# Kernel optimization log

Measured on AMD Instinct MI355X. Metric: run time of the kernel, lower is better.

The kernel has to match this reference:

```python
import jax, jax.numpy as jnp
import numpy as np

N_HEAD = 8  # heads; per-head scores are summed before softmax


def setup_inputs() -> dict:
    key = jax.random.key(0)
    k1, k2, k3 = jax.random.split(key, 3)
    B, T, D = 4, 512, 1024
    N, H = 16, 256  # n_concepts, init_size
    x = jax.random.normal(k1, (B, T, D), dtype=jnp.float32)
    # original init: kaiming_uniform then / d_model**2 -> very small weights; plain normal scaled similarly
    w_qs = jax.random.normal(k2, (N, D, H), dtype=jnp.float32) / (D ** 1.0)
    w_ks = jax.random.normal(k3, (N, D, H), dtype=jnp.float32) / (D ** 1.0)
    return {"x": x, "w_qs": w_qs, "w_ks": w_ks}


def reference(x, w_qs, w_ks):
    # x: [B,T,D]; w_qs/w_ks: [N,D,H]
    # Faithful to source: k_list is built from wq (source bug), so scores = q.q^T; w_ks unused in math.
    wq = jnp.einsum('btd,ndh->bnth', x, w_qs)  # [B,N,T,H]
    # Per-head split then sum over heads of q_h @ k_h^T equals the full-H contraction
    # (mask is None), so fuse: sum_h qk_h == wq @ wq^T over the whole H axis.
    attn = jnp.einsum('bnsh,bnth->bnst', wq, wq)  # temperature = 1.0; head-sum fused
    attn = jax.nn.softmax(attn, axis=-1)  # [B,N,T,T]
    # input = x.unsqueeze(1): [B,1,T,D]; einsum 'bnst,bitd->bnsd' broadcasts i=1
    e_aggregated = jnp.einsum('bnst,btd->bnsd', attn, x)  # [B,N,T,D]
    return e_aggregated, attn
```

## Files before the change

kernel.cpp:

```cpp
#include <hip/hip_runtime.h>
#include <hip/hip_bf16.h>

typedef __bf16 bf16x8 __attribute__((ext_vector_type(8)));
typedef unsigned short u16x8 __attribute__((ext_vector_type(8)));
typedef float f32x4 __attribute__((ext_vector_type(4)));
typedef __hip_bfloat16 hbf;

static constexpr int B = 4, T = 512, D = 1024, N = 16, H = 256;
static constexpr size_t E_ELEMS = (size_t)B * N * T * D;
static constexpr size_t ATTN_ELEMS = (size_t)B * N * T * T;

__device__ __forceinline__ bf16x8 load8(const hbf* p) {
  return *reinterpret_cast<const bf16x8*>(p);
}

__device__ __forceinline__ unsigned short f2bf(float f) {
  union { __hip_bfloat16 h; unsigned short u; } cv;
  cv.h = __float2bfloat16(f);
  return cv.u;
}

__device__ __forceinline__ void gload16(const hbf* g, hbf* l) {
  __builtin_amdgcn_global_load_lds(
      (const __attribute__((address_space(1))) void*)g,
      (__attribute__((address_space(3))) void*)l, 16, 0, 0);
}

__global__ __launch_bounds__(256) void cast_bf_k(const float* __restrict__ in,
                                                 unsigned short* __restrict__ out,
                                                 int n8) {
  int i = blockIdx.x * 256 + threadIdx.x;
  if (i >= n8) return;
  const float4* p = reinterpret_cast<const float4*>(in) + (size_t)i * 2;
  float4 a = p[0], b = p[1];
  u16x8 v;
  v[0] = f2bf(a.x); v[1] = f2bf(a.y); v[2] = f2bf(a.z); v[3] = f2bf(a.w);
  v[4] = f2bf(b.x); v[5] = f2bf(b.y); v[6] = f2bf(b.z); v[7] = f2bf(b.w);
  reinterpret_cast<u16x8*>(out)[i] = v;
}

__global__ void transpose_cast_k(const float* __restrict__ in,
                                 unsigned short* __restrict__ out, int R, int C) {
  __shared__ unsigned short tile[32][33];
  int z = blockIdx.z;
  int c0 = blockIdx.x * 32, r0 = blockIdx.y * 32;
  const float* inz = in + (size_t)z * R * C;
  unsigned short* outz = out + (size_t)z * R * C;
  int tx = threadIdx.x, ty = threadIdx.y;
  for (int i = ty; i < 32; i += 8)
    tile[i][tx] = f2bf(inz[(size_t)(r0 + i) * C + (c0 + tx)]);
  __syncthreads();
  for (int i = ty; i < 32; i += 8)
    outz[(size_t)(c0 + i) * R + (r0 + tx)] = tile[tx][i];
}

__global__ __launch_bounds__(256) void gemm_wq_tiled(const hbf* __restrict__ xb,
                                                     const hbf* __restrict__ wT,
                                                     hbf* __restrict__ wq) {
  __shared__ __align__(16) hbf As[128 * 32];
  __shared__ __align__(16) hbf Bs[128 * 32];
  int idx = blockIdx.x;
  int b = idx >> 7, mt = (idx >> 5) & 3, jt = idx & 31;
  const hbf* A = xb + (size_t)b * T * D + (size_t)mt * 128 * D;
  const hbf* Bp = wT + (size_t)jt * 128 * D;
  int tid = threadIdx.x, wave = tid >> 6, lane = tid & 63;
  int col = lane & 15, quad = lane >> 4;
  int wm = wave & 1, wn = wave >> 1;
  const hbf* stG = (wave < 2) ? A : Bp;
  hbf* stL = (wave < 2) ? As : Bs;
  int ibase = (wave & 1) * 4;
  f32x4 acc[4][4] = {};
  for (int k0 = 0; k0 < D; k0 += 32) {
    __syncthreads();
#pragma unroll
    for (int j = 0; j < 4; ++j) {
      int slot = (ibase + j) * 64 + lane;
      int row = slot >> 2, kc = slot & 3;
      gload16(stG + (size_t)row * D + k0 + kc * 8, stL + slot * 8);
    }
    __syncthreads();
    bf16x8 a[4], bb[4];
#pragma unroll
    for (int s = 0; s < 4; ++s)
      a[s] = load8(As + (wm * 64 + s * 16 + col) * 32 + quad * 8);
#pragma unroll
    for (int t = 0; t < 4; ++t)
      bb[t] = load8(Bs + (wn * 64 + t * 16 + col) * 32 + quad * 8);
#pragma unroll
    for (int s = 0; s < 4; ++s)
#pragma unroll
      for (int t = 0; t < 4; ++t)
        acc[s][t] = __builtin_amdgcn_mfma_f32_16x16x32_bf16(a[s], bb[t], acc[s][t], 0, 0, 0);
  }
  hbf* wqb = wq + (size_t)b * 16 * T * H;
#pragma unroll
  for (int s = 0; s < 4; ++s) {
    int row = mt * 128 + wm * 64 + s * 16 + quad * 4;
#pragma unroll
    for (int t = 0; t < 4; ++t) {
      int j = jt * 128 + wn * 64 + t * 16 + col;
      int n = j >> 8, h = j & 255;
      hbf* dst = wqb + (size_t)n * T * H + (size_t)row * H + h;
#pragma unroll
      for (int r = 0; r < 4; ++r)
        dst[(size_t)r * H] = __float2bfloat16(acc[s][t][r]);
    }
  }
}

__global__ __launch_bounds__(256) void attn_k(const hbf* __restrict__ wq,
                                              float* __restrict__ attn_f,
                                              hbf* __restrict__ attn_b) {
  __shared__ float S[16][516];
  int blk = blockIdx.x;
  int bn = blk >> 5;
  int mt = blk & 31;
  const hbf* Wq = wq + (size_t)bn * T * H;
  int wave = threadIdx.x >> 6, lane = threadIdx.x & 63;
  int col = lane & 15, quad = lane >> 4;
  int m0 = mt * 16;
  f32x4 acc[8] = {};
  for (int k0 = 0; k0 < H; k0 += 32) {
    int k = k0 + quad * 8;
    bf16x8 afrag = load8(Wq + (size_t)(m0 + col) * H + k);
#pragma unroll
    for (int t = 0; t < 8; ++t) {
      int jrow = wave * 128 + t * 16 + col;
      bf16x8 bfrag = load8(Wq + (size_t)jrow * H + k);
      acc[t] = __builtin_amdgcn_mfma_f32_16x16x32_bf16(afrag, bfrag, acc[t], 0, 0, 0);
    }
  }
#pragma unroll
  for (int t = 0; t < 8; ++t)
#pragma unroll
    for (int r = 0; r < 4; ++r)
      S[quad * 4 + r][wave * 128 + t * 16 + col] = acc[t][r];
  __syncthreads();
  for (int rr = 0; rr < 4; ++rr) {
    int row = wave * 4 + rr;
    float v[8];
    float mx = -1e30f;
#pragma unroll
    for (int i = 0; i < 8; ++i) { v[i] = S[row][lane + i * 64]; mx = fmaxf(mx, v[i]); }
#pragma unroll
    for (int off = 32; off > 0; off >>= 1) mx = fmaxf(mx, __shfl_xor(mx, off));
    float sum = 0.f;
#pragma unroll
    for (int i = 0; i < 8; ++i) { v[i] = __expf(v[i] - mx); sum += v[i]; }
#pragma unroll
    for (int off = 32; off > 0; off >>= 1) sum += __shfl_xor(sum, off);
    float inv = 1.0f / sum;
    size_t base = ((size_t)bn * T + m0 + row) * T;
    float* dst = attn_f + base;
    hbf* dstb = attn_b + base;
#pragma unroll
    for (int i = 0; i < 8; ++i) {
      float p = v[i] * inv;
      dst[lane + i * 64] = p;
      dstb[lane + i * 64] = __float2bfloat16(p);
    }
  }
}

__global__ __launch_bounds__(256) void gemm_out_tiled(const hbf* __restrict__ attn,
                                                      const hbf* __restrict__ xT,
                                                      float* __restrict__ eout) {
  __shared__ __align__(16) hbf As[128 * 32];
  __shared__ __align__(16) hbf Bs[128 * 32];
  int idx = blockIdx.x;
  int bn = idx >> 5, mt = (idx >> 3) & 3, nt = idx & 7;
  int b = bn >> 4;
  const hbf* A = attn + (size_t)bn * T * T + (size_t)mt * 128 * T;
  const hbf* Bp = xT + (size_t)b * D * T + (size_t)nt * 128 * T;
  float* C = eout + (size_t)bn * T * D;
  int tid = threadIdx.x, wave = tid >> 6, lane = tid & 63;
  int col = lane & 15, quad = lane >> 4;
  int wm = wave & 1, wn = wave >> 1;
  const hbf* stG = (wave < 2) ? A : Bp;
  hbf* stL = (wave < 2) ? As : Bs;
  int ibase = (wave & 1) * 4;
  f32x4 acc[4][4] = {};
  for (int k0 = 0; k0 < T; k0 += 32) {
    __syncthreads();
#pragma unroll
    for (int j = 0; j < 4; ++j) {
      int slot = (ibase + j) * 64 + lane;
      int row = slot >> 2, kc = slot & 3;
      gload16(stG + (size_t)row * T + k0 + kc * 8, stL + slot * 8);
    }
    __syncthreads();
    bf16x8 a[4], bb[4];
#pragma unroll
    for (int s = 0; s < 4; ++s)
      a[s] = load8(As + (wm * 64 + s * 16 + col) * 32 + quad * 8);
#pragma unroll
    for (int t = 0; t < 4; ++t)
      bb[t] = load8(Bs + (wn * 64 + t * 16 + col) * 32 + quad * 8);
#pragma unroll
    for (int s = 0; s < 4; ++s)
#pragma unroll
      for (int t = 0; t < 4; ++t)
        acc[s][t] = __builtin_amdgcn_mfma_f32_16x16x32_bf16(a[s], bb[t], acc[s][t], 0, 0, 0);
  }
#pragma unroll
  for (int s = 0; s < 4; ++s) {
    int row = mt * 128 + wm * 64 + s * 16 + quad * 4;
#pragma unroll
    for (int t = 0; t < 4; ++t) {
      int d = nt * 128 + wn * 64 + t * 16 + col;
      float* dst = C + (size_t)row * D + d;
#pragma unroll
      for (int r = 0; r < 4; ++r)
        dst[(size_t)r * D] = acc[s][t][r];
    }
  }
}

extern "C" void kernel_launch(void* const* d_in, const int* in_sizes, int n_in,
                              void* d_out, int out_size, void* d_ws, size_t ws_size,
                              hipStream_t stream) {
  const float* x = (const float*)d_in[0];
  const float* w_qs = (const float*)d_in[1];
  float* e_out = (float*)d_out;
  float* attn_out = e_out + E_ELEMS;

  char* ws = (char*)d_ws;
  hbf* x_bf = (hbf*)ws;
  hbf* xT   = (hbf*)(ws + (4u << 20));
  hbf* wT   = (hbf*)(ws + (8u << 20));
  hbf* wq   = (hbf*)(ws + (16u << 20));
  hbf* attn_b = (hbf*)(ws + (32u << 20));

  dim3 tb(32, 8);
  cast_bf_k<<<1024, 256, 0, stream>>>(x, (unsigned short*)x_bf, (B * T * D) / 8);
  transpose_cast_k<<<dim3(H / 32, D / 32, N), tb, 0, stream>>>(
      w_qs, (unsigned short*)wT, D, H);
  transpose_cast_k<<<dim3(D / 32, T / 32, B), tb, 0, stream>>>(
      x, (unsigned short*)xT, T, D);
  gemm_wq_tiled<<<512, 256, 0, stream>>>(x_bf, wT, wq);
  attn_k<<<2048, 256, 0, stream>>>(wq, attn_out, attn_b);
  gemm_out_tiled<<<2048, 256, 0, stream>>>(attn_b, xT, e_out);
}
```

Before: 364.9 us.

## Fuse softmax attention with PV matmul, keeping probabilities in swizzled LDS

Merges the score/softmax kernel and the attn@x GEMM into one kernel. Each block computes 32 query rows, runs the softmax in registers with cross-wave reductions through shared memory, and keeps the bf16 probabilities in XOR-swizzled LDS, then multiplies them by xT streamed straight from global memory. This removes the bf16 attention round trip through global memory and one launch. In exchange, the PV stage reads B fragments directly from global without LDS staging and uses fewer, heavier blocks with a 32KB LDS footprint.

```diff
diff --git a/kernel.cpp b/kernel.cpp
--- a/kernel.cpp
+++ b/kernel.cpp
@@ -108,111 +108,122 @@
   }
 }
 
-__global__ __launch_bounds__(256) void attn_k(const hbf* __restrict__ wq,
-                                              float* __restrict__ attn_f,
-                                              hbf* __restrict__ attn_b) {
-  __shared__ float S[16][516];
+__global__ __launch_bounds__(256) void attn_pv_fused(
+    const hbf* __restrict__ wq, const hbf* __restrict__ xT,
+    float* __restrict__ attn_f, float* __restrict__ eout) {
+  __shared__ __align__(16) char Pl[32 * 512 * 2];
+  __shared__ float redA[4][32];
+  __shared__ float redB[4][32];
   int blk = blockIdx.x;
-  int bn = blk >> 5;
-  int mt = blk & 31;
+  int bn = blk >> 4, mt = blk & 15;
+  int b = bn >> 4;
+  int m0 = mt * 32;
   const hbf* Wq = wq + (size_t)bn * T * H;
   int wave = threadIdx.x >> 6, lane = threadIdx.x & 63;
   int col = lane & 15, quad = lane >> 4;
-  int m0 = mt * 16;
-  f32x4 acc[8] = {};
+
+  f32x4 acc[2][8] = {};
   for (int k0 = 0; k0 < H; k0 += 32) {
     int k = k0 + quad * 8;
-    bf16x8 afrag = load8(Wq + (size_t)(m0 + col) * H + k);
+    bf16x8 af[2];
+#pragma unroll
+    for (int s = 0; s < 2; ++s)
+      af[s] = load8(Wq + (size_t)(m0 + s * 16 + col) * H + k);
 #pragma unroll
     for (int t = 0; t < 8; ++t) {
-      int jrow = wave * 128 + t * 16 + col;
-      bf16x8 bfrag = load8(Wq + (size_t)jrow * H + k);
-      acc[t] = __builtin_amdgcn_mfma_f32_16x16x32_bf16(afrag, bfrag, acc[t], 0, 0, 0);
-    }
-  }
-#pragma unroll
-  for (int t = 0; t < 8; ++t)
-#pragma unroll
-    for (int r = 0; r < 4; ++r)
-      S[quad * 4 + r][wave * 128 + t * 16 + col] = acc[t][r];
-  __syncthreads();
-  for (int rr = 0; rr < 4; ++rr) {
-    int row = wave * 4 + rr;
-    float v[8];
-    float mx = -1e30f;
-#pragma unroll
-    for (int i = 0; i < 8; ++i) { v[i] = S[row][lane + i * 64]; mx = fmaxf(mx, v[i]); }
-#pragma unroll
-    for (int off = 32; off > 0; off >>= 1) mx = fmaxf(mx, __shfl_xor(mx, off));
-    float sum = 0.f;
-#pragma unroll
-    for (int i = 0; i < 8; ++i) { v[i] = __expf(v[i] - mx); sum += v[i]; }
-#pragma unroll
-    for (int off = 32; off > 0; off >>= 1) sum += __shfl_xor(sum, off);
-    float inv = 1.0f / sum;
-    size_t base = ((size_t)bn * T + m0 + row) * T;
-    float* dst = attn_f + base;
-    hbf* dstb = attn_b + base;
-#pragma unroll
-    for (int i = 0; i < 8; ++i) {
-      float p = v[i] * inv;
-      dst[lane + i * 64] = p;
-      dstb[lane + i * 64] = __float2bfloat16(p);
-    }
-  }
-}
-
-__global__ __launch_bounds__(256) void gemm_out_tiled(const hbf* __restrict__ attn,
-                                                      const hbf* __restrict__ xT,
-                                                      float* __restrict__ eout) {
-  __shared__ __align__(16) hbf As[128 * 32];
-  __shared__ __align__(16) hbf Bs[128 * 32];
-  int idx = blockIdx.x;
-  int bn = idx >> 5, mt = (idx >> 3) & 3, nt = idx & 7;
-  int b = bn >> 4;
-  const hbf* A = attn + (size_t)bn * T * T + (size_t)mt * 128 * T;
-  const hbf* Bp = xT + (size_t)b * D * T + (size_t)nt * 128 * T;
-  float* C = eout + (size_t)bn * T * D;
-  int tid = threadIdx.x, wave = tid >> 6, lane = tid & 63;
-  int col = lane & 15, quad = lane >> 4;
-  int wm = wave & 1, wn = wave >> 1;
-  const hbf* stG = (wave < 2) ? A : Bp;
-  hbf* stL = (wave < 2) ? As : Bs;
-  int ibase = (wave & 1) * 4;
-  f32x4 acc[4][4] = {};
-  for (int k0 = 0; k0 < T; k0 += 32) {
-    __syncthreads();
-#pragma unroll
-    for (int j = 0; j < 4; ++j) {
-      int slot = (ibase + j) * 64 + lane;
-      int row = slot >> 2, kc = slot & 3;
-      gload16(stG + (size_t)row * T + k0 + kc * 8, stL + slot * 8);
-    }
-    __syncthreads();
-    bf16x8 a[4], bb[4];
-#pragma unroll
-    for (int s = 0; s < 4; ++s)
-      a[s] = load8(As + (wm * 64 + s * 16 + col) * 32 + quad * 8);
-#pragma unroll
-    for (int t = 0; t < 4; ++t)
-      bb[t] = load8(Bs + (wn * 64 + t * 16 + col) * 32 + quad * 8);
-#pragma unroll
-    for (int s = 0; s < 4; ++s)
-#pragma unroll
-      for (int t = 0; t < 4; ++t)
-        acc[s][t] = __builtin_amdgcn_mfma_f32_16x16x32_bf16(a[s], bb[t], acc[s][t], 0, 0, 0);
-  }
-#pragma unroll
-  for (int s = 0; s < 4; ++s) {
-    int row = mt * 128 + wm * 64 + s * 16 + quad * 4;
-#pragma unroll
-    for (int t = 0; t < 4; ++t) {
-      int d = nt * 128 + wn * 64 + t * 16 + col;
-      float* dst = C + (size_t)row * D + d;
-#pragma unroll
-      for (int r = 0; r < 4; ++r)
-        dst[(size_t)r * D] = acc[s][t][r];
-    }
+      bf16x8 bfr = load8(Wq + (size_t)(wave * 128 + t * 16 + col) * H + k);
+#pragma unroll
+      for (int s = 0; s < 2; ++s)
+        acc[s][t] = __builtin_amdgcn_mfma_f32_16x16x32_bf16(af[s], bfr, acc[s][t], 0, 0, 0);
+    }
+  }
+
+  float mrow[2][4], inv[2][4];
+#pragma unroll
+  for (int s = 0; s < 2; ++s)
+#pragma unroll
+    for (int r = 0; r < 4; ++r) {
+      float pm = acc[s][0][r];
+#pragma unroll
+      for (int t = 1; t < 8; ++t) pm = fmaxf(pm, acc[s][t][r]);
+#pragma unroll
+      for (int off = 8; off >= 1; off >>= 1) pm = fmaxf(pm, __shfl_xor(pm, off));
+      if (col == 0) redA[wave][s * 16 + quad * 4 + r] = pm;
+    }
+  __syncthreads();
+#pragma unroll
+  for (int s = 0; s < 2; ++s)
+#pragma unroll
+    for (int r = 0; r < 4; ++r) {
+      int rl = s * 16 + quad * 4 + r;
+      mrow[s][r] = fmaxf(fmaxf(redA[0][rl], redA[1][rl]),
+                         fmaxf(redA[2][rl], redA[3][rl]));
+      float sm = 0.f;
+#pragma unroll
+      for (int t = 0; t < 8; ++t) {
+        float e = __expf(acc[s][t][r] - mrow[s][r]);
+        acc[s][t][r] = e;
+        sm += e;
+      }
+#pragma unroll
+      for (int off = 8; off >= 1; off >>= 1) sm += __shfl_xor(sm, off);
+      if (col == 0) redB[wave][rl] = sm;
+    }
+  __syncthreads();
+#pragma unroll
+  for (int s = 0; s < 2; ++s)
+#pragma unroll
+    for (int r = 0; r < 4; ++r) {
+      int rl = s * 16 + quad * 4 + r;
+      inv[s][r] = 1.0f / (redB[0][rl] + redB[1][rl] + redB[2][rl] + redB[3][rl]);
+    }
+#pragma unroll
+  for (int s = 0; s < 2; ++s)
+#pragma unroll
+    for (int r = 0; r < 4; ++r) {
+      int rl = s * 16 + quad * 4 + r;
+      float iv = inv[s][r];
+      float* dst = attn_f + ((size_t)bn * T + m0 + rl) * T;
+#pragma unroll
+      for (int t = 0; t < 8; ++t) {
+        int c = wave * 128 + t * 16 + col;
+        float p = acc[s][t][r] * iv;
+        dst[c] = p;
+        int byte = ((rl * 512 + c) * 2) ^ ((rl & 7) << 4);
+        *reinterpret_cast<hbf*>(Pl + byte) = __float2bfloat16(p);
+      }
+    }
+  __syncthreads();
+
+  const hbf* xTb = xT + (size_t)b * D * T;
+  float* Cc = eout + ((size_t)bn * T + m0) * D;
+  for (int h = 0; h < 2; ++h) {
+    int dbase = wave * 256 + h * 128;
+    f32x4 a3[2][8] = {};
+    for (int k0 = 0; k0 < T; k0 += 32) {
+      int k = k0 + quad * 8;
+      bf16x8 pf[2];
+#pragma unroll
+      for (int s = 0; s < 2; ++s) {
+        int row = s * 16 + col;
+        int byte = ((row * 512 + k) * 2) ^ ((row & 7) << 4);
+        pf[s] = *reinterpret_cast<const bf16x8*>(Pl + byte);
+      }
+#pragma unroll
+      for (int t = 0; t < 8; ++t) {
+        bf16x8 bfr = load8(xTb + (size_t)(dbase + t * 16 + col) * T + k);
+#pragma unroll
+        for (int s = 0; s < 2; ++s)
+          a3[s][t] = __builtin_amdgcn_mfma_f32_16x16x32_bf16(pf[s], bfr, a3[s][t], 0, 0, 0);
+      }
+    }
+#pragma unroll
+    for (int s = 0; s < 2; ++s)
+#pragma unroll
+      for (int t = 0; t < 8; ++t)
+#pragma unroll
+        for (int r = 0; r < 4; ++r)
+          Cc[(size_t)(s * 16 + quad * 4 + r) * D + dbase + t * 16 + col] = a3[s][t][r];
   }
 }
 
@@ -229,7 +240,6 @@
   hbf* xT   = (hbf*)(ws + (4u << 20));
   hbf* wT   = (hbf*)(ws + (8u << 20));
   hbf* wq   = (hbf*)(ws + (16u << 20));
-  hbf* attn_b = (hbf*)(ws + (32u << 20));
 
   dim3 tb(32, 8);
   cast_bf_k<<<1024, 256, 0, stream>>>(x, (unsigned short*)x_bf, (B * T * D) / 8);
@@ -238,6 +248,5 @@
   transpose_cast_k<<<dim3(D / 32, T / 32, B), tb, 0, stream>>>(
       x, (unsigned short*)xT, T, D);
   gemm_wq_tiled<<<512, 256, 0, stream>>>(x_bf, wT, wq);
-  attn_k<<<2048, 256, 0, stream>>>(wq, attn_out, attn_b);
-  gemm_out_tiled<<<2048, 256, 0, stream>>>(attn_b, xT, e_out);
-}
+  attn_pv_fused<<<1024, 256, 0, stream>>>(wq, xT, attn_out, e_out);
+}
```

New measurement: 513.3 us. +40.7%, slower.

## Triple-buffer LDS staging in both tiled GEMMs with async prefetch

Applied to the files above, without the earlier changes.

Both tiled bf16 GEMMs (x·W projection and attn·x output) move from a single LDS buffer with two barriers per k-step to a three-stage ring. Tiles k+1 and k+2 are fetched with global_load_lds while tile k is computed, and explicit vmcnt waits plus one barrier per iteration replace the old double syncthreads. The goal is to hide global load latency behind MFMA work. It triples LDS use per block, which may lower occupancy, and correctness depends on the hand-set vmcnt counts matching the number of outstanding loads.

```diff
diff --git a/kernel.cpp b/kernel.cpp
--- a/kernel.cpp
+++ b/kernel.cpp
@@ -57,8 +57,8 @@
 __global__ __launch_bounds__(256) void gemm_wq_tiled(const hbf* __restrict__ xb,
                                                      const hbf* __restrict__ wT,
                                                      hbf* __restrict__ wq) {
-  __shared__ __align__(16) hbf As[128 * 32];
-  __shared__ __align__(16) hbf Bs[128 * 32];
+  __shared__ __align__(16) hbf As[3][128 * 32];
+  __shared__ __align__(16) hbf Bs[3][128 * 32];
   int idx = blockIdx.x;
   int b = idx >> 7, mt = (idx >> 5) & 3, jt = idx & 31;
   const hbf* A = xb + (size_t)b * T * D + (size_t)mt * 128 * D;
@@ -67,25 +67,37 @@
   int col = lane & 15, quad = lane >> 4;
   int wm = wave & 1, wn = wave >> 1;
   const hbf* stG = (wave < 2) ? A : Bp;
-  hbf* stL = (wave < 2) ? As : Bs;
   int ibase = (wave & 1) * 4;
-  f32x4 acc[4][4] = {};
-  for (int k0 = 0; k0 < D; k0 += 32) {
-    __syncthreads();
+
+  auto STAGE = [&](int kt, int bi) {
+    hbf* stL = (wave < 2) ? As[bi] : Bs[bi];
 #pragma unroll
     for (int j = 0; j < 4; ++j) {
       int slot = (ibase + j) * 64 + lane;
       int row = slot >> 2, kc = slot & 3;
-      gload16(stG + (size_t)row * D + k0 + kc * 8, stL + slot * 8);
-    }
-    __syncthreads();
+      gload16(stG + (size_t)row * D + kt * 32 + kc * 8, stL + slot * 8);
+    }
+  };
+
+  f32x4 acc[4][4] = {};
+  constexpr int NT = D / 32;
+  STAGE(0, 0);
+  STAGE(1, 1);
+  for (int k = 0; k < NT; ++k) {
+    int cb = k % 3;
+    if (k == NT - 1)
+      asm volatile("s_waitcnt vmcnt(0)" ::: "memory");
+    else
+      asm volatile("s_waitcnt vmcnt(4)" ::: "memory");
+    __builtin_amdgcn_s_barrier();
+    if (k + 2 < NT) STAGE(k + 2, (k + 2) % 3);
     bf16x8 a[4], bb[4];
 #pragma unroll
     for (int s = 0; s < 4; ++s)
-      a[s] = load8(As + (wm * 64 + s * 16 + col) * 32 + quad * 8);
+      a[s] = load8(As[cb] + (wm * 64 + s * 16 + col) * 32 + quad * 8);
 #pragma unroll
     for (int t = 0; t < 4; ++t)
-      bb[t] = load8(Bs + (wn * 64 + t * 16 + col) * 32 + quad * 8);
+      bb[t] = load8(Bs[cb] + (wn * 64 + t * 16 + col) * 32 + quad * 8);
 #pragma unroll
     for (int s = 0; s < 4; ++s)
 #pragma unroll
@@ -165,8 +177,8 @@
 __global__ __launch_bounds__(256) void gemm_out_tiled(const hbf* __restrict__ attn,
                                                       const hbf* __restrict__ xT,
                                                       float* __restrict__ eout) {
-  __shared__ __align__(16) hbf As[128 * 32];
-  __shared__ __align__(16) hbf Bs[128 * 32];
+  __shared__ __align__(16) hbf As[3][128 * 32];
+  __shared__ __align__(16) hbf Bs[3][128 * 32];
   int idx = blockIdx.x;
   int bn = idx >> 5, mt = (idx >> 3) & 3, nt = idx & 7;
   int b = bn >> 4;
@@ -177,25 +189,37 @@
   int col = lane & 15, quad = lane >> 4;
   int wm = wave & 1, wn = wave >> 1;
   const hbf* stG = (wave < 2) ? A : Bp;
-  hbf* stL = (wave < 2) ? As : Bs;
   int ibase = (wave & 1) * 4;
-  f32x4 acc[4][4] = {};
-  for (int k0 = 0; k0 < T; k0 += 32) {
-    __syncthreads();
+
+  auto STAGE = [&](int kt, int bi) {
+    hbf* stL = (wave < 2) ? As[bi] : Bs[bi];
 #pragma unroll
     for (int j = 0; j < 4; ++j) {
       int slot = (ibase + j) * 64 + lane;
       int row = slot >> 2, kc = slot & 3;
-      gload16(stG + (size_t)row * T + k0 + kc * 8, stL + slot * 8);
-    }
-    __syncthreads();
+      gload16(stG + (size_t)row * T + kt * 32 + kc * 8, stL + slot * 8);
+    }
+  };
+
+  f32x4 acc[4][4] = {};
+  constexpr int NT = T / 32;
+  STAGE(0, 0);
+  STAGE(1, 1);
+  for (int k = 0; k < NT; ++k) {
+    int cb = k % 3;
+    if (k == NT - 1)
+      asm volatile("s_waitcnt vmcnt(0)" ::: "memory");
+    else
+      asm volatile("s_waitcnt vmcnt(4)" ::: "memory");
+    __builtin_amdgcn_s_barrier();
+    if (k + 2 < NT) STAGE(k + 2, (k + 2) % 3);
     bf16x8 a[4], bb[4];
 #pragma unroll
     for (int s = 0; s < 4; ++s)
-      a[s] = load8(As + (wm * 64 + s * 16 + col) * 32 + quad * 8);
+      a[s] = load8(As[cb] + (wm * 64 + s * 16 + col) * 32 + quad * 8);
 #pragma unroll
     for (int t = 0; t < 4; ++t)
-      bb[t] = load8(Bs + (wn * 64 + t * 16 + col) * 32 + quad * 8);
+      bb[t] = load8(Bs[cb] + (wn * 64 + t * 16 + col) * 32 + quad * 8);
 #pragma unroll
     for (int s = 0; s < 4; ++s)
 #pragma unroll
```

After: 362.2 us. About the same (-0.7%).
